# Performance work log

Hardware: AMD Instinct MI355X
Metric: run time of the kernel (lower is better)

Reference implementation:

```python
import jax, jax.numpy as jnp
import numpy as np

B, V, NB, NJ, NEXTRA = 512, 6890, 10, 24, 9
PARENTS = np.array([-1,0,0,0,1,2,3,4,5,6,7,8,9,9,9,12,13,14,16,17,18,19,20,21], dtype=np.int32)


def setup_inputs() -> dict:
    key = jax.random.key(0)
    ks = jax.random.split(key, 11)
    betas = jax.random.normal(ks[0], (B, NB + 1), jnp.float32) * 0.1
    betas = betas.at[:, 0].set(1.0)  # col 0 is a global scale in this SMPL variant
    body_pose = jax.random.normal(ks[1], (B, 3 * (NJ - 1)), jnp.float32) * 0.2
    global_orient = jax.random.normal(ks[2], (B, 3), jnp.float32) * 0.2
    transl = jax.random.normal(ks[3], (B, 3), jnp.float32) * 0.1
    model_scale_opt = jnp.ones((1,), jnp.float32)
    smpl_v_template = jax.random.normal(ks[4], (V, 3), jnp.float32)
    smil_v_template = jax.random.normal(ks[5], (V, 3), jnp.float32)
    shapedirs = jax.random.normal(ks[6], (V, 3, NB), jnp.float32) * 0.01
    J_regressor = jax.nn.softmax(jax.random.normal(ks[7], (NJ, V), jnp.float32), axis=1)
    lbs_weights = jax.nn.softmax(jax.random.normal(ks[8], (V, NJ), jnp.float32) * 4.0, axis=1)
    J_regressor_extra = jax.nn.softmax(jax.random.normal(ks[9], (NEXTRA, V), jnp.float32), axis=1)
    parents = jnp.asarray(PARENTS)
    return dict(betas=betas, body_pose=body_pose, global_orient=global_orient,
                transl=transl, model_scale_opt=model_scale_opt,
                smpl_v_template=smpl_v_template, smil_v_template=smil_v_template,
                shapedirs=shapedirs, J_regressor=J_regressor, lbs_weights=lbs_weights,
                J_regressor_extra=J_regressor_extra, parents=parents)


def batch_rodrigues(rvecs):
    # rvecs: [N,3] axis-angle -> [N,3,3] rotation matrices
    angle = jnp.linalg.norm(rvecs + 1e-8, axis=1, keepdims=True)  # [N,1]
    axis = rvecs / angle
    c = jnp.cos(angle)[..., None]  # [N,1,1]
    s = jnp.sin(angle)[..., None]
    rx, ry, rz = axis[:, 0], axis[:, 1], axis[:, 2]
    z = jnp.zeros_like(rx)
    K = jnp.stack([z, -rz, ry, rz, z, -rx, -ry, rx, z], axis=1).reshape(-1, 3, 3)
    I = jnp.eye(3, dtype=rvecs.dtype)
    return I + s * K + (1.0 - c) * jnp.matmul(K, K)


def _smpl_forward(betas, body_pose, global_orient, transl, model_scale_opt,
                  smpl_v_template, smil_v_template, shapedirs,
                  J_regressor, lbs_weights, J_regressor_extra):
    dtype = betas.dtype
    # ---- updateShape ----
    s = model_scale_opt[0]
    v_template = smpl_v_template * s + (1.0 - s) * smil_v_template  # [V,3]
    blend_shape = jnp.einsum('bl,mkl->bmk', betas[:, 1:], shapedirs)  # [B,V,3]
    v_shaped = (v_template[None] + blend_shape) * betas[:, :1, None]  # scale col
    J_shaped = jnp.einsum('bik,ji->bjk', v_shaped, J_regressor)  # [B,NJ,3]

    # ---- updatePose ----
    full_pose = jnp.concatenate([global_orient, body_pose], axis=1)  # [B,NJ*3]
    rot_mats = batch_rodrigues(full_pose.reshape(-1, 3)).reshape(B, NJ, 3, 3)

    # relative joint locations w.r.t. parents
    rel_joints = J_shaped.at[:, 1:].add(-J_shaped[:, PARENTS[1:]])
    top = jnp.concatenate([rot_mats, rel_joints[..., None]], axis=-1)  # [B,NJ,3,4]
    bottom = jnp.broadcast_to(
        jnp.array([0.0, 0.0, 0.0, 1.0], dtype=dtype), (B, NJ, 1, 4))
    mats = jnp.concatenate([top, bottom], axis=2)  # [B,NJ,4,4]

    # sequential kinematic-chain composition over the 24-joint tree
    chain = [mats[:, 0]]
    for i in range(1, NJ):
        chain.append(jnp.matmul(chain[PARENTS[i]], mats[:, i]))
    chain = jnp.stack(chain, axis=1)  # [B,NJ,4,4]
    posed_joints = chain[:, :, :3, 3]  # [B,NJ,3]

    # relative transforms: subtract rotated rest joints
    corr = jnp.einsum('bjmn,bjn->bjm', chain[:, :, :3, :3], J_shaped)
    A = chain.at[:, :, :3, 3].add(-corr)  # [B,NJ,4,4]

    # linear blend skinning
    T = jnp.einsum('vj,bjmn->bvmn', lbs_weights, A)  # [B,V,4,4]
    verts = jnp.einsum('bvmn,bvn->bvm', T[:, :, :3, :3], v_shaped) + T[:, :, :3, 3]

    extra_joints = jnp.einsum('bik,ji->bjk', verts, J_regressor_extra)  # [B,9,3]
    joints = jnp.concatenate([posed_joints, extra_joints], axis=1)  # [B,33,3]

    t = transl[:, None, :]
    # concat verts and joints along point dim for a single output array
    return jnp.concatenate([verts + t, joints + t], axis=1)  # [B, V+33, 3]


def reference(betas, body_pose, global_orient, transl, model_scale_opt,
              smpl_v_template, smil_v_template, shapedirs,
              J_regressor, lbs_weights, J_regressor_extra, parents):
    return _smpl_forward(betas, body_pose, global_orient, transl, model_scale_opt,
                         smpl_v_template, smil_v_template, shapedirs,
                         J_regressor, lbs_weights, J_regressor_extra)
```

## Files before the change

### kernel.cpp

```cpp
#include <hip/hip_runtime.h>


#define BATCH 512
#define NV 6890
#define NBD 10
#define NJ 24
#define NEXTRA 9
#define NOUT (NV + NJ + NEXTRA)
#define VBLK ((NV + 255) / 256)
#define BPB 4

__constant__ int c_par[NJ] = {-1,0,0,0,1,2,3,4,5,6,7,8,9,9,9,12,13,14,16,17,18,19,20,21};

__global__ __launch_bounds__(256) void precompute_kernel(
    const float* __restrict__ jreg,
    const float* __restrict__ smpl_t,
    const float* __restrict__ smil_t,
    const float* __restrict__ sdirs,
    const float* __restrict__ msc,
    float* __restrict__ jtjs)
{
    const int j = blockIdx.y;
    const int v = blockIdx.x * 256 + threadIdx.x;
    const float s = msc[0];

    float acc[33];
#pragma unroll
    for (int i = 0; i < 33; ++i) acc[i] = 0.f;

    if (v < NV) {
        const float w = jreg[j * NV + v];
#pragma unroll
        for (int k = 0; k < 3; ++k) {
            float vt = s * smpl_t[v * 3 + k] + (1.f - s) * smil_t[v * 3 + k];
            acc[k] = w * vt;
        }
        const float2* sd2 = (const float2*)(sdirs + (size_t)v * 30);
#pragma unroll
        for (int i = 0; i < 15; ++i) {
            float2 x = sd2[i];
            acc[3 + 2 * i]     = w * x.x;
            acc[3 + 2 * i + 1] = w * x.y;
        }
    }

#pragma unroll
    for (int i = 0; i < 33; ++i) {
        float x = acc[i];
        for (int off = 32; off; off >>= 1) x += __shfl_xor(x, off, 64);
        acc[i] = x;
    }

    __shared__ float red[4][33];
    const int lane = threadIdx.x & 63, wv = threadIdx.x >> 6;
    if (lane == 0) {
#pragma unroll
        for (int i = 0; i < 33; ++i) red[wv][i] = acc[i];
    }
    __syncthreads();
    if (threadIdx.x < 33) {
        float sum = red[0][threadIdx.x] + red[1][threadIdx.x]
                  + red[2][threadIdx.x] + red[3][threadIdx.x];
        atomicAdd(&jtjs[j * 33 + threadIdx.x], sum);
    }
}

__global__ __launch_bounds__(64) void joints_kernel(
    const float* __restrict__ betas,
    const float* __restrict__ body_pose,
    const float* __restrict__ glob_or,
    const float* __restrict__ transl,
    const float* __restrict__ jtjs,
    float* __restrict__ wsA,
    float* __restrict__ out)
{
    const int b = blockIdx.x;
    const int j = threadIdx.x;

    __shared__ float sJ[NJ][3];
    __shared__ float mats[NJ][12];
    __shared__ float chain[NJ][12];
    __shared__ float sbeta[NBD + 1];

    if (threadIdx.x < NBD + 1) sbeta[threadIdx.x] = betas[b * (NBD + 1) + threadIdx.x];
    __syncthreads();

    if (j < NJ) {
        const float beta0 = sbeta[0];
#pragma unroll
        for (int k = 0; k < 3; ++k) {
            float a = jtjs[j * 33 + k];
#pragma unroll
            for (int l = 0; l < NBD; ++l) a = fmaf(sbeta[1 + l], jtjs[j * 33 + 3 + k * 10 + l], a);
            sJ[j][k] = a * beta0;
        }
        float rx, ry, rz;
        if (j == 0) {
            rx = glob_or[b * 3 + 0]; ry = glob_or[b * 3 + 1]; rz = glob_or[b * 3 + 2];
        } else {
            rx = body_pose[b * 69 + (j - 1) * 3 + 0];
            ry = body_pose[b * 69 + (j - 1) * 3 + 1];
            rz = body_pose[b * 69 + (j - 1) * 3 + 2];
        }
        float ex = rx + 1e-8f, ey = ry + 1e-8f, ez = rz + 1e-8f;
        float ang = sqrtf(ex * ex + ey * ey + ez * ez);
        float inv = 1.f / ang;
        float ax = rx * inv, ay = ry * inv, az = rz * inv;
        float c = cosf(ang), s = sinf(ang), t = 1.f - c;
        mats[j][0]  = 1.f + t * (-(ay * ay + az * az));
        mats[j][1]  = -s * az + t * (ax * ay);
        mats[j][2]  =  s * ay + t * (ax * az);
        mats[j][4]  =  s * az + t * (ax * ay);
        mats[j][5]  = 1.f + t * (-(ax * ax + az * az));
        mats[j][6]  = -s * ax + t * (ay * az);
        mats[j][8]  = -s * ay + t * (ax * az);
        mats[j][9]  =  s * ax + t * (ay * az);
        mats[j][10] = 1.f + t * (-(ax * ax + ay * ay));
    }
    __syncthreads();
    if (j < NJ) {
        const int p = c_par[j];
        float t0 = sJ[j][0], t1 = sJ[j][1], t2 = sJ[j][2];
        if (p >= 0) { t0 -= sJ[p][0]; t1 -= sJ[p][1]; t2 -= sJ[p][2]; }
        mats[j][3] = t0; mats[j][7] = t1; mats[j][11] = t2;
    }
    __syncthreads();
    if (threadIdx.x == 0) {
#pragma unroll
        for (int k = 0; k < 12; ++k) chain[0][k] = mats[0][k];
        for (int i = 1; i < NJ; ++i) {
            const int p = c_par[i];
#pragma unroll
            for (int r = 0; r < 3; ++r) {
#pragma unroll
                for (int col = 0; col < 4; ++col) {
                    float acc = (col == 3) ? chain[p][r * 4 + 3] : 0.f;
#pragma unroll
                    for (int q = 0; q < 3; ++q) acc = fmaf(chain[p][r * 4 + q], mats[i][q * 4 + col], acc);
                    chain[i][r * 4 + col] = acc;
                }
            }
        }
    }
    __syncthreads();
    if (j < NJ) {
        float A[12];
#pragma unroll
        for (int k = 0; k < 12; ++k) A[k] = chain[j][k];
        const float c0 = A[3], c1 = A[7], c2 = A[11];
        const float j0 = sJ[j][0], j1 = sJ[j][1], j2 = sJ[j][2];
        A[3]  = c0 - (A[0] * j0 + A[1] * j1 + A[2]  * j2);
        A[7]  = c1 - (A[4] * j0 + A[5] * j1 + A[6]  * j2);
        A[11] = c2 - (A[8] * j0 + A[9] * j1 + A[10] * j2);
#pragma unroll
        for (int k = 0; k < 12; ++k) wsA[((size_t)b * NJ + j) * 12 + k] = A[k];
        const float tx = transl[b * 3 + 0], ty = transl[b * 3 + 1], tz = transl[b * 3 + 2];
        const size_t o = ((size_t)b * NOUT + NV + j) * 3;
        out[o + 0] = c0 + tx; out[o + 1] = c1 + ty; out[o + 2] = c2 + tz;
    }
}

__global__ __launch_bounds__(256) void lbs_kernel(
    const float* __restrict__ betas,
    const float* __restrict__ transl,
    const float* __restrict__ msc,
    const float* __restrict__ smpl_t,
    const float* __restrict__ smil_t,
    const float* __restrict__ sdirs,
    const float* __restrict__ lbsw,
    const float* __restrict__ wsA,
    float* __restrict__ out)
{
    const int v = blockIdx.x * 256 + threadIdx.x;
    const bool valid = v < NV;
    const int vc = valid ? v : NV - 1;
    const int b0 = blockIdx.y * BPB;
    const float s = msc[0];

    float vt[3];
#pragma unroll
    for (int k = 0; k < 3; ++k)
        vt[k] = s * smpl_t[vc * 3 + k] + (1.f - s) * smil_t[vc * 3 + k];

    float sd[30];
    {
        const float2* sd2 = (const float2*)(sdirs + (size_t)vc * 30);
#pragma unroll
        for (int i = 0; i < 15; ++i) { float2 x = sd2[i]; sd[2 * i] = x.x; sd[2 * i + 1] = x.y; }
    }
    float w[NJ];
    {
        const float4* w4 = (const float4*)(lbsw + (size_t)vc * NJ);
#pragma unroll
        for (int i = 0; i < 6; ++i) {
            float4 x = w4[i];
            w[4 * i] = x.x; w[4 * i + 1] = x.y; w[4 * i + 2] = x.z; w[4 * i + 3] = x.w;
        }
    }

#pragma unroll
    for (int bb = 0; bb < BPB; ++bb) {
        const int b = b0 + bb;
        const float* __restrict__ Bb = betas + b * (NBD + 1);
        const float* __restrict__ Ab = wsA + (size_t)b * NJ * 12;

        float vs[3];
#pragma unroll
        for (int k = 0; k < 3; ++k) {
            float a = vt[k];
#pragma unroll
            for (int l = 0; l < NBD; ++l) a = fmaf(Bb[1 + l], sd[k * 10 + l], a);
            vs[k] = a * Bb[0];
        }

        float T[12];
#pragma unroll
        for (int k = 0; k < 12; ++k) T[k] = 0.f;
#pragma unroll 4
        for (int jj = 0; jj < NJ; ++jj) {
            const float ww = w[jj];
#pragma unroll
            for (int k = 0; k < 12; ++k) T[k] = fmaf(ww, Ab[jj * 12 + k], T[k]);
        }

        if (valid) {
            const float tx = transl[b * 3 + 0], ty = transl[b * 3 + 1], tz = transl[b * 3 + 2];
            const size_t o = ((size_t)b * NOUT + v) * 3;
            out[o + 0] = fmaf(T[0], vs[0], fmaf(T[1], vs[1], fmaf(T[2],  vs[2], T[3])))  + tx;
            out[o + 1] = fmaf(T[4], vs[0], fmaf(T[5], vs[1], fmaf(T[6],  vs[2], T[7])))  + ty;
            out[o + 2] = fmaf(T[8], vs[0], fmaf(T[9], vs[1], fmaf(T[10], vs[2], T[11]))) + tz;
        }
    }
}

__global__ __launch_bounds__(256) void extra_kernel(
    const float* __restrict__ jre,
    float* out)
{
    const int b = blockIdx.x;
    const float* vb = out + (size_t)b * NOUT * 3;

    float acc[27];
#pragma unroll
    for (int i = 0; i < 27; ++i) acc[i] = 0.f;

    for (int v = threadIdx.x; v < NV; v += 256) {
        const float x = vb[v * 3 + 0], y = vb[v * 3 + 1], z = vb[v * 3 + 2];
#pragma unroll
        for (int e = 0; e < NEXTRA; ++e) {
            const float we = jre[e * NV + v];
            acc[e * 3 + 0] = fmaf(we, x, acc[e * 3 + 0]);
            acc[e * 3 + 1] = fmaf(we, y, acc[e * 3 + 1]);
            acc[e * 3 + 2] = fmaf(we, z, acc[e * 3 + 2]);
        }
    }

#pragma unroll
    for (int i = 0; i < 27; ++i) {
        float x = acc[i];
        for (int off = 32; off; off >>= 1) x += __shfl_xor(x, off, 64);
        acc[i] = x;
    }
    __shared__ float red[4][27];
    const int lane = threadIdx.x & 63, wv = threadIdx.x >> 6;
    if (lane == 0) {
#pragma unroll
        for (int i = 0; i < 27; ++i) red[wv][i] = acc[i];
    }
    __syncthreads();
    if (threadIdx.x < 27) {
        const float sum = red[0][threadIdx.x] + red[1][threadIdx.x]
                        + red[2][threadIdx.x] + red[3][threadIdx.x];
        out[((size_t)b * NOUT + NV + NJ) * 3 + threadIdx.x] = sum;
    }
}

extern "C" void kernel_launch(void* const* d_in, const int* in_sizes, int n_in,
                              void* d_out, int out_size, void* d_ws, size_t ws_size,
                              hipStream_t stream) {
    const float* betas     = (const float*)d_in[0];
    const float* body_pose = (const float*)d_in[1];
    const float* glob_or   = (const float*)d_in[2];
    const float* transl    = (const float*)d_in[3];
    const float* msc       = (const float*)d_in[4];
    const float* smpl_t    = (const float*)d_in[5];
    const float* smil_t    = (const float*)d_in[6];
    const float* sdirs     = (const float*)d_in[7];
    const float* jreg      = (const float*)d_in[8];
    const float* lbsw      = (const float*)d_in[9];
    const float* jre       = (const float*)d_in[10];

    float* out  = (float*)d_out;
    float* ws   = (float*)d_ws;
    float* jtjs = ws;
    float* wsA  = ws + 792;

    hipMemsetAsync(jtjs, 0, NJ * 33 * sizeof(float), stream);

    dim3 gA(VBLK, NJ);
    precompute_kernel<<<gA, 256, 0, stream>>>(jreg, smpl_t, smil_t, sdirs, msc, jtjs);

    joints_kernel<<<BATCH, 64, 0, stream>>>(betas, body_pose, glob_or, transl, jtjs, wsA, out);

    dim3 gC(VBLK, BATCH / BPB);
    lbs_kernel<<<gC, 256, 0, stream>>>(betas, transl, msc, smpl_t, smil_t, sdirs, lbsw, wsA, out);

    extra_kernel<<<BATCH, 256, 0, stream>>>(jre, out);
}
```

Baseline: 187.6 us.

## Stage joint transforms in LDS, split extra-joint reduction, drop precompute atomics

The LBS kernel now loads the per-batch joint transforms into shared memory once per block and fully unrolls the joint loop, instead of reading them from global memory per thread. The extra-joint regression is split into four vertex chunks per batch and combined with atomics, and joints_kernel zero-initialises the target slots. The shape precompute uses one block per joint with a strided loop, which removes the memset and the global atomics. The cost is extra synchronisation and shared memory, fewer blocks in precompute, and float-atomic nondeterminism in the extra joints.

```diff
diff --git a/kernel.cpp b/kernel.cpp
--- a/kernel.cpp
+++ b/kernel.cpp
@@ -9,6 +9,7 @@
 #define NOUT (NV + NJ + NEXTRA)
 #define VBLK ((NV + 255) / 256)
 #define BPB 4
+#define ECHUNK ((NV + 3) / 4)
 
 __constant__ int c_par[NJ] = {-1,0,0,0,1,2,3,4,5,6,7,8,9,9,9,12,13,14,16,17,18,19,20,21};
 
@@ -20,27 +21,26 @@
     const float* __restrict__ msc,
     float* __restrict__ jtjs)
 {
-    const int j = blockIdx.y;
-    const int v = blockIdx.x * 256 + threadIdx.x;
+    const int j = blockIdx.x;
     const float s = msc[0];
 
     float acc[33];
 #pragma unroll
     for (int i = 0; i < 33; ++i) acc[i] = 0.f;
 
-    if (v < NV) {
+    for (int v = threadIdx.x; v < NV; v += 256) {
         const float w = jreg[j * NV + v];
 #pragma unroll
         for (int k = 0; k < 3; ++k) {
             float vt = s * smpl_t[v * 3 + k] + (1.f - s) * smil_t[v * 3 + k];
-            acc[k] = w * vt;
+            acc[k] = fmaf(w, vt, acc[k]);
         }
         const float2* sd2 = (const float2*)(sdirs + (size_t)v * 30);
 #pragma unroll
         for (int i = 0; i < 15; ++i) {
             float2 x = sd2[i];
-            acc[3 + 2 * i]     = w * x.x;
-            acc[3 + 2 * i + 1] = w * x.y;
+            acc[3 + 2 * i]     = fmaf(w, x.x, acc[3 + 2 * i]);
+            acc[3 + 2 * i + 1] = fmaf(w, x.y, acc[3 + 2 * i + 1]);
         }
     }
 
@@ -59,9 +59,8 @@
     }
     __syncthreads();
     if (threadIdx.x < 33) {
-        float sum = red[0][threadIdx.x] + red[1][threadIdx.x]
-                  + red[2][threadIdx.x] + red[3][threadIdx.x];
-        atomicAdd(&jtjs[j * 33 + threadIdx.x], sum);
+        jtjs[j * 33 + threadIdx.x] = red[0][threadIdx.x] + red[1][threadIdx.x]
+                                   + red[2][threadIdx.x] + red[3][threadIdx.x];
     }
 }
 
@@ -83,6 +82,10 @@
     __shared__ float sbeta[NBD + 1];
 
     if (threadIdx.x < NBD + 1) sbeta[threadIdx.x] = betas[b * (NBD + 1) + threadIdx.x];
+
+    if (threadIdx.x >= NJ && threadIdx.x < NJ + 3 * NEXTRA)
+        out[((size_t)b * NOUT + NV + NJ) * 3 + (threadIdx.x - NJ)] = 0.f;
+
     __syncthreads();
 
     if (j < NJ) {
@@ -171,10 +174,21 @@
     const float* __restrict__ wsA,
     float* __restrict__ out)
 {
-    const int v = blockIdx.x * 256 + threadIdx.x;
+    __shared__ float sA[BPB][NJ * 12];
+
+    const int tid = threadIdx.x;
+    const int b0 = blockIdx.y * BPB;
+
+    {
+        const float4* src = (const float4*)(wsA + (size_t)b0 * NJ * 12);
+        float4* dst = (float4*)&sA[0][0];
+        if (tid < 256)      dst[tid] = src[tid];
+        if (tid < BPB * NJ * 12 / 4 - 256) dst[tid + 256] = src[tid + 256];
+    }
+
+    const int v = blockIdx.x * 256 + tid;
     const bool valid = v < NV;
     const int vc = valid ? v : NV - 1;
-    const int b0 = blockIdx.y * BPB;
     const float s = msc[0];
 
     float vt[3];
@@ -198,11 +212,13 @@
         }
     }
 
+    __syncthreads();
+
 #pragma unroll
     for (int bb = 0; bb < BPB; ++bb) {
         const int b = b0 + bb;
         const float* __restrict__ Bb = betas + b * (NBD + 1);
-        const float* __restrict__ Ab = wsA + (size_t)b * NJ * 12;
+        const float* Ab = sA[bb];
 
         float vs[3];
 #pragma unroll
@@ -216,7 +232,7 @@
         float T[12];
 #pragma unroll
         for (int k = 0; k < 12; ++k) T[k] = 0.f;
-#pragma unroll 4
+#pragma unroll
         for (int jj = 0; jj < NJ; ++jj) {
             const float ww = w[jj];
 #pragma unroll
@@ -237,14 +253,16 @@
     const float* __restrict__ jre,
     float* out)
 {
-    const int b = blockIdx.x;
+    const int b = blockIdx.y;
+    const int v0 = blockIdx.x * ECHUNK;
+    int vend = v0 + ECHUNK; if (vend > NV) vend = NV;
     const float* vb = out + (size_t)b * NOUT * 3;
 
     float acc[27];
 #pragma unroll
     for (int i = 0; i < 27; ++i) acc[i] = 0.f;
 
-    for (int v = threadIdx.x; v < NV; v += 256) {
+    for (int v = v0 + threadIdx.x; v < vend; v += 256) {
         const float x = vb[v * 3 + 0], y = vb[v * 3 + 1], z = vb[v * 3 + 2];
 #pragma unroll
         for (int e = 0; e < NEXTRA; ++e) {
@@ -271,7 +289,7 @@
     if (threadIdx.x < 27) {
         const float sum = red[0][threadIdx.x] + red[1][threadIdx.x]
                         + red[2][threadIdx.x] + red[3][threadIdx.x];
-        out[((size_t)b * NOUT + NV + NJ) * 3 + threadIdx.x] = sum;
+        atomicAdd(&out[((size_t)b * NOUT + NV + NJ) * 3 + threadIdx.x], sum);
     }
 }
 
@@ -295,15 +313,13 @@
     float* jtjs = ws;
     float* wsA  = ws + 792;
 
-    hipMemsetAsync(jtjs, 0, NJ * 33 * sizeof(float), stream);
-
-    dim3 gA(VBLK, NJ);
-    precompute_kernel<<<gA, 256, 0, stream>>>(jreg, smpl_t, smil_t, sdirs, msc, jtjs);
+    precompute_kernel<<<NJ, 256, 0, stream>>>(jreg, smpl_t, smil_t, sdirs, msc, jtjs);
 
     joints_kernel<<<BATCH, 64, 0, stream>>>(betas, body_pose, glob_or, transl, jtjs, wsA, out);
 
     dim3 gC(VBLK, BATCH / BPB);
     lbs_kernel<<<gC, 256, 0, stream>>>(betas, transl, msc, smpl_t, smil_t, sdirs, lbsw, wsA, out);
 
-    extra_kernel<<<BATCH, 256, 0, stream>>>(jre, out);
-}
+    dim3 gE(4, BATCH);
+    extra_kernel<<<gE, 256, 0, stream>>>(jre, out);
+}
```

Measured after the change: 256.8 us. +36.9%, slower.
